# Kernel tuning notes

Measured on AMD Instinct MI355X. Metric: run time of the kernel, lower is better.

The kernel has to match this reference:

```python
import jax, jax.numpy as jnp
import numpy as np

NEG_SLOPE = 0.2
EPS = 1e-16

def gat_conv(x, edge_index, W, a_src, a_dst, b):
    # x: [N, Fin], W: [Fin, C], a_src/a_dst: [C], b: [C]
    N = x.shape[0]
    src, dst = edge_index[0], edge_index[1]
    h = x @ W                                  # [N, C]
    alpha_s = h @ a_src                        # [N]
    alpha_d = h @ a_dst                        # [N]
    e = alpha_s[src] + alpha_d[dst]            # [E]
    e = jnp.where(e > 0, e, NEG_SLOPE * e)     # LeakyReLU(0.2)
    # ragged softmax over incoming edges of each dst node
    m = jax.ops.segment_max(e, dst, num_segments=N)       # [N]
    p = jnp.exp(e - m[dst])                                # [E]
    s = jax.ops.segment_sum(p, dst, num_segments=N)        # [N]
    alpha = p / (s[dst] + EPS)                             # [E]
    out = jax.ops.segment_sum(alpha[:, None] * h[src], dst, num_segments=N)
    return out + b

def setup_inputs() -> dict:
    key = jax.random.key(0)
    ks = jax.random.split(key, 10)
    N, Fin, H, C, E = 50000, 128, 64, 64, 800000
    x = jax.random.normal(ks[0], (N, Fin), dtype=jnp.float32)
    edge_index = jax.random.randint(ks[1], (2, E), 0, N, dtype=jnp.int64)
    sc1 = 1.0 / np.sqrt(Fin)
    sc2 = 1.0 / np.sqrt(H)
    W1 = jax.random.normal(ks[2], (Fin, H), dtype=jnp.float32) * sc1
    a_src1 = jax.random.normal(ks[3], (H,), dtype=jnp.float32) * sc2
    a_dst1 = jax.random.normal(ks[4], (H,), dtype=jnp.float32) * sc2
    b1 = jnp.zeros((H,), dtype=jnp.float32)
    W2 = jax.random.normal(ks[5], (H, C), dtype=jnp.float32) * sc2
    a_src2 = jax.random.normal(ks[6], (C,), dtype=jnp.float32) * sc2
    a_dst2 = jax.random.normal(ks[7], (C,), dtype=jnp.float32) * sc2
    b2 = jnp.zeros((C,), dtype=jnp.float32)
    return {"x": x, "edge_index": edge_index, "W1": W1, "a_src1": a_src1,
            "a_dst1": a_dst1, "b1": b1, "W2": W2, "a_src2": a_src2,
            "a_dst2": a_dst2, "b2": b2}

def reference(x, edge_index, W1, a_src1, a_dst1, b1, W2, a_src2, a_dst2, b2):
    h = gat_conv(x, edge_index, W1, a_src1, a_dst1, b1)
    h = jax.nn.relu(h)
    out = gat_conv(h, edge_index, W2, a_src2, a_dst2, b2)
    return out
```

## Files before the change

### kernel.cpp

```cpp
#include <hip/hip_runtime.h>
#include <cstddef>

constexpr int FIN = 128;
constexpr int EPB = 2048;
constexpr int BSH = 7;
constexpr int NPB = 128;
constexpr int PACK_SH = 25;
constexpr int SRCMASK = (1 << PACK_SH) - 1;
constexpr int RSTR = 512;
constexpr int CAP = 4608;
constexpr int RPS = NPB + 1;

typedef _Float16 half4 __attribute__((ext_vector_type(4)));
typedef _Float16 half8 __attribute__((ext_vector_type(8)));
typedef float floatx4 __attribute__((ext_vector_type(4)));

template <int NW>
__device__ __forceinline__ int block_scan_tot(int v, int tid, int* wsums,
                                              int* tot) {
    int lane = tid & 63, w = tid >> 6;
    int x = v;
#pragma unroll
    for (int off = 1; off < 64; off <<= 1) {
        int y = __shfl_up(x, off, 64);
        if (lane >= off) x += y;
    }
    if (lane == 63) wsums[w] = x;
    __syncthreads();
    int add = 0, t = 0;
#pragma unroll
    for (int i = 0; i < NW; ++i) {
        add += (i < w) ? wsums[i] : 0;
        t += wsums[i];
    }
    *tot = t;
    return x + add - v;
}

template <int K>
__device__ __forceinline__
void gemm_core(const float* __restrict__ W, const float* __restrict__ ASRC,
               const float* __restrict__ ADST, _Float16* __restrict__ Hh,
               float* __restrict__ AS, float* __restrict__ AD, int N, int nb,
               _Float16* Xh, _Float16* WT) {
    constexpr int LDH = K + 8;
    const int tid = threadIdx.x;
    for (int i = tid; i < 64 * (K / 4); i += 256) {
        int n = i & 63, kg = i >> 6;
        half4 h;
#pragma unroll
        for (int j = 0; j < 4; ++j)
            h[j] = (_Float16)W[(4 * kg + j) * 64 + n];
        *(half4*)(WT + n * LDH + 4 * kg) = h;
    }
    __syncthreads();

    const int l = tid & 63;
    const int r0 = (tid >> 6) * 16;
    const int n16 = l & 15, quad = l >> 4;

    floatx4 acc[4];
#pragma unroll
    for (int nt = 0; nt < 4; ++nt) acc[nt] = (floatx4){0.f, 0.f, 0.f, 0.f};

#pragma unroll
    for (int k0 = 0; k0 < K; k0 += 32) {
        half8 a = *(const half8*)(Xh + (r0 + n16) * LDH + k0 + quad * 8);
#pragma unroll
        for (int nt = 0; nt < 4; ++nt) {
            half8 b = *(const half8*)(WT + (nt * 16 + n16) * LDH + k0 + quad * 8);
            acc[nt] = __builtin_amdgcn_mfma_f32_16x16x32_f16(a, b, acc[nt], 0, 0, 0);
        }
    }

    float pa[4] = {0.f, 0.f, 0.f, 0.f}, pd[4] = {0.f, 0.f, 0.f, 0.f};
#pragma unroll
    for (int nt = 0; nt < 4; ++nt) {
        float as_v = ASRC[nt * 16 + n16], ad_v = ADST[nt * 16 + n16];
#pragma unroll
        for (int reg = 0; reg < 4; ++reg) {
            pa[reg] += acc[nt][reg] * as_v;
            pd[reg] += acc[nt][reg] * ad_v;
        }
    }
#pragma unroll
    for (int off = 1; off < 16; off <<= 1) {
#pragma unroll
        for (int reg = 0; reg < 4; ++reg) {
            pa[reg] += __shfl_xor(pa[reg], off, 64);
            pd[reg] += __shfl_xor(pd[reg], off, 64);
        }
    }
    if (n16 == 0) {
#pragma unroll
        for (int reg = 0; reg < 4; ++reg) {
            int row = nb + r0 + quad * 4 + reg;
            if (row < N) { AS[row] = pa[reg]; AD[row] = pd[reg]; }
        }
    }

#pragma unroll
    for (int nt = 0; nt < 4; ++nt)
#pragma unroll
        for (int reg = 0; reg < 4; ++reg)
            Xh[(r0 + quad * 4 + reg) * LDH + nt * 16 + n16] = (_Float16)acc[nt][reg];
    {
        int r = r0 + (l >> 2);
        int o = (l & 3) * 16;
        if (nb + r < N) {
            half8 v0 = *(const half8*)(Xh + r * LDH + o);
            half8 v1 = *(const half8*)(Xh + r * LDH + o + 8);
            *(half8*)(Hh + (size_t)(nb + r) * 64 + o) = v0;
            *(half8*)(Hh + (size_t)(nb + r) * 64 + o + 8) = v1;
        }
    }
}

template <int K, typename XT>
__device__ __forceinline__
void gemm_mfma_body(const XT* __restrict__ X, const float* __restrict__ W,
                    const float* __restrict__ ASRC, const float* __restrict__ ADST,
                    _Float16* __restrict__ Hh, float* __restrict__ AS,
                    float* __restrict__ AD, int N, int blk,
                    _Float16* Xh, _Float16* WT) {
    constexpr int LDH = K + 8;
    const int tid = threadIdx.x;
    const int nb = blk * 64;
    if constexpr (sizeof(XT) == 4) {
        constexpr int QPR = K / 4;
        for (int i = tid; i < 64 * QPR; i += 256) {
            int r = i / QPR, q = i % QPR;
            float4 v = make_float4(0.f, 0.f, 0.f, 0.f);
            if (nb + r < N) v = *(const float4*)(X + (size_t)(nb + r) * K + 4 * q);
            half4 h; h[0] = (_Float16)v.x; h[1] = (_Float16)v.y;
            h[2] = (_Float16)v.z; h[3] = (_Float16)v.w;
            *(half4*)(Xh + r * LDH + 4 * q) = h;
        }
    } else {
        constexpr int OPR = K / 8;
        for (int i = tid; i < 64 * OPR; i += 256) {
            int r = i / OPR, o = i % OPR;
            half8 v = {};
            if (nb + r < N) v = *(const half8*)(X + (size_t)(nb + r) * K + 8 * o);
            *(half8*)(Xh + r * LDH + 8 * o) = v;
        }
    }
    gemm_core<K>(W, ASRC, ADST, Hh, AS, AD, N, nb, Xh, WT);
}

__global__ __launch_bounds__(256)
void gemm1_and_sort(const float* __restrict__ X, const float* __restrict__ W,
                    const float* __restrict__ ASRC, const float* __restrict__ ADST,
                    _Float16* __restrict__ Hh, float* __restrict__ AS,
                    float* __restrict__ AD, int N,
                    const int* __restrict__ src, const int* __restrict__ dst,
                    int E, int nblk, int nbuck,
                    int* __restrict__ rows, int* __restrict__ ebuck) {
    constexpr int K = FIN, LDH = K + 8;
    __shared__ _Float16 Xh[64 * LDH];
    __shared__ _Float16 WT[64 * LDH];
    __shared__ int wsums[4];

    const int tid = threadIdx.x;
    if ((int)blockIdx.x < nblk) {
        int* sorted = (int*)Xh;
        int* hist   = (int*)WT;
        int* cur    = hist + 512;
        for (int i = tid; i < nbuck; i += 256) hist[i] = 0;
        __syncthreads();

        const int e0 = blockIdx.x * EPB;
        const int e1 = min(e0 + EPB, E);
        const int cnt = e1 - e0;

        int pay[8], bk[8];
#pragma unroll
        for (int k = 0; k < 8; ++k) {
            int e = e0 + tid + k * 256;
            bk[k] = -1; pay[k] = 0;
            if (e < e1) {
                int d = dst[e];
                bk[k] = d >> BSH;
                pay[k] = ((d & (NPB - 1)) << PACK_SH) | src[e];
                atomicAdd(&hist[bk[k]], 1);
            }
        }
        __syncthreads();

        int i0 = 2 * tid, i1 = 2 * tid + 1;
        int v0 = (i0 < nbuck) ? hist[i0] : 0;
        int v1 = (i1 < nbuck) ? hist[i1] : 0;
        int tot;
        int ex = block_scan_tot<4>(v0 + v1, tid, wsums, &tot);
        if (i0 < nbuck) {
            cur[i0] = ex;
            rows[blockIdx.x * RSTR + i0] = ex;
        }
        if (i1 < nbuck) {
            cur[i1] = ex + v0;
            rows[blockIdx.x * RSTR + i1] = ex + v0;
        }
        if (tid == 0) rows[blockIdx.x * RSTR + nbuck] = cnt;
        __syncthreads();

#pragma unroll
        for (int k = 0; k < 8; ++k) {
            if (bk[k] >= 0) {
                int p = atomicAdd(&cur[bk[k]], 1);
                sorted[p] = pay[k];
            }
        }
        __syncthreads();
        for (int i = tid; i < cnt; i += 256)
            ebuck[blockIdx.x * EPB + i] = sorted[i];
        return;
    }
    gemm_mfma_body<K, float>(X, W, ASRC, ADST, Hh, AS, AD, N,
                             blockIdx.x - nblk, Xh, WT);
}

template <int K, typename XT>
__global__ __launch_bounds__(256)
void gemm_feat(const XT* __restrict__ X, const float* __restrict__ W,
               const float* __restrict__ ASRC, const float* __restrict__ ADST,
               _Float16* __restrict__ Hh, float* __restrict__ AS,
               float* __restrict__ AD, int N) {
    constexpr int LDH = K + 8;
    __shared__ _Float16 Xh[64 * LDH];
    __shared__ _Float16 WT[64 * LDH];
    gemm_mfma_body<K, XT>(X, W, ASRC, ADST, Hh, AS, AD, N, blockIdx.x, Xh, WT);
}

template <typename OT>
__device__ __forceinline__
void agg_one_node(const _Float16* __restrict__ Hh, const float* __restrict__ AS,
                  const float* __restrict__ AD, const int* __restrict__ csr_src,
                  const float* __restrict__ bias, OT* __restrict__ OUT,
                  int n, int base, int end, int lane, int relu) {
    const int cnt = end - base;
    const float adn = AD[n];

    if (cnt > 64) {
        float m = -INFINITY;
        for (int c0 = base; c0 < end; c0 += 64) {
            int c = min(64, end - c0);
            float e = -INFINITY;
            if (lane < c) {
                int sr = csr_src[c0 + lane];
                float t = AS[sr] + adn;
                e = t > 0.f ? t : 0.2f * t;
            }
#pragma unroll
            for (int off = 32; off > 0; off >>= 1) e = fmaxf(e, __shfl_xor(e, off, 64));
            m = fmaxf(m, e);
        }
        float s = 0.f, acc = 0.f;
        for (int c0 = base; c0 < end; c0 += 64) {
            int c = min(64, end - c0);
            int srcl = 0;
            float p = 0.f;
            if (lane < c) {
                srcl = csr_src[c0 + lane];
                float t = AS[srcl] + adn;
                t = t > 0.f ? t : 0.2f * t;
                p = __expf(t - m);
            }
            float cs = p;
#pragma unroll
            for (int off = 32; off > 0; off >>= 1) cs += __shfl_xor(cs, off, 64);
            s += cs;
            for (int j = 0; j < c; ++j)
                acc += __shfl(p, j, 64) *
                       (float)Hh[(size_t)__shfl(srcl, j, 64) * 64 + lane];
        }
        float o = acc * (1.f / (s + 1e-16f)) + bias[lane];
        if (relu) o = fmaxf(o, 0.f);
        OUT[(size_t)n * 64 + lane] = (OT)o;
        return;
    }

    int srcl = 0;
    float el = 0.f;
    if (lane < cnt) {
        srcl = csr_src[base + lane];
        float e = AS[srcl] + adn;
        el = e > 0.f ? e : 0.2f * e;
    }
    float p = (lane < cnt) ? __expf(el) : 0.f;
    float s = p;
#pragma unroll
    for (int off = 32; off > 0; off >>= 1) s += __shfl_xor(s, off, 64);
    const float inv = 1.f / (s + 1e-16f);

    const int eg = lane >> 3;
    const int c8 = (lane & 7) * 8;

    float acc[8], acc2[8];
#pragma unroll
    for (int t = 0; t < 8; ++t) { acc[t] = 0.f; acc2[t] = 0.f; }

    int j = 0;
    for (; j + 16 <= cnt; j += 16) {
        int iA = j + eg, iB = j + 8 + eg;
        int sA = __shfl(srcl, iA, 64), sB = __shfl(srcl, iB, 64);
        float aA = __shfl(p, iA, 64),  aB = __shfl(p, iB, 64);
        half8 hA = *(const half8*)(Hh + (size_t)sA * 64 + c8);
        half8 hB = *(const half8*)(Hh + (size_t)sB * 64 + c8);
#pragma unroll
        for (int t = 0; t < 8; ++t) {
            acc[t]  += aA * (float)hA[t];
            acc2[t] += aB * (float)hB[t];
        }
    }
    for (; j < cnt; j += 8) {
        int iA = j + eg;
        int sA = __shfl(srcl, iA, 64);
        float aA = __shfl(p, iA, 64);
        half8 hA = *(const half8*)(Hh + (size_t)sA * 64 + c8);
#pragma unroll
        for (int t = 0; t < 8; ++t) acc[t] += aA * (float)hA[t];
    }
#pragma unroll
    for (int t = 0; t < 8; ++t) acc[t] += acc2[t];
#pragma unroll
    for (int off = 8; off <= 32; off <<= 1)
#pragma unroll
        for (int t = 0; t < 8; ++t) acc[t] += __shfl_xor(acc[t], off, 64);

    if (lane < 8) {
        float4 b0 = *(const float4*)(bias + c8);
        float4 b1 = *(const float4*)(bias + c8 + 4);
        float o[8];
        o[0] = acc[0] * inv + b0.x; o[1] = acc[1] * inv + b0.y;
        o[2] = acc[2] * inv + b0.z; o[3] = acc[3] * inv + b0.w;
        o[4] = acc[4] * inv + b1.x; o[5] = acc[5] * inv + b1.y;
        o[6] = acc[6] * inv + b1.z; o[7] = acc[7] * inv + b1.w;
        if (relu) {
#pragma unroll
            for (int t = 0; t < 8; ++t) o[t] = fmaxf(o[t], 0.f);
        }
        if constexpr (sizeof(OT) == 2) {
            half8 hv;
#pragma unroll
            for (int t = 0; t < 8; ++t) hv[t] = (_Float16)o[t];
            *(half8*)((_Float16*)OUT + (size_t)n * 64 + c8) = hv;
        } else {
            *(float4*)((float*)OUT + (size_t)n * 64 + c8) =
                make_float4(o[0], o[1], o[2], o[3]);
            *(float4*)((float*)OUT + (size_t)n * 64 + c8 + 4) =
                make_float4(o[4], o[5], o[6], o[7]);
        }
    }
}

template <typename OT>
__device__ __forceinline__
void agg_pair_core(const _Float16* __restrict__ Hh, const float* __restrict__ AS,
                   const float* __restrict__ AD, const int* __restrict__ csr,
                   const float* __restrict__ bias, OT* __restrict__ OUT,
                   int n, int N, int relu, int lane, int base, int end) {
    const int l32 = lane & 31;
    const int cnt = end - base;

    if (!__all(cnt <= 32)) {
        int baseA = __shfl(base, 0, 64),  endA = __shfl(end, 0, 64);
        int baseB = __shfl(base, 32, 64), endB = __shfl(end, 32, 64);
        int nA = __shfl(n, 0, 64), nB = __shfl(n, 32, 64);
        if (nA < N) agg_one_node<OT>(Hh, AS, AD, csr, bias, OUT, nA, baseA, endA, lane, relu);
        if (nB < N) agg_one_node<OT>(Hh, AS, AD, csr, bias, OUT, nB, baseB, endB, lane, relu);
        return;
    }

    const float adn = (n < N) ? AD[n] : 0.f;
    int srcl = 0;
    float p = 0.f;
    if (l32 < cnt) {
        srcl = csr[base + l32];
        float e = AS[srcl] + adn;
        e = e > 0.f ? e : 0.2f * e;
        p = __expf(e);
    }
    float s = p;
#pragma unroll
    for (int off = 16; off > 0; off >>= 1) s += __shfl_xor(s, off, 64);
    const float inv = 1.f / (s + 1e-16f);

    const int eg = l32 >> 3;
    const int c8 = (l32 & 7) * 8;

    float acc[8], acc2[8];
#pragma unroll
    for (int t = 0; t < 8; ++t) { acc[t] = 0.f; acc2[t] = 0.f; }

    int j = 0;
    for (; j + 8 <= cnt; j += 8) {
        int iA = j + eg, iB = j + 4 + eg;
        int sA = __shfl(srcl, iA, 32), sB = __shfl(srcl, iB, 32);
        float aA = __shfl(p, iA, 32),  aB = __shfl(p, iB, 32);
        half8 hA = *(const half8*)(Hh + (size_t)sA * 64 + c8);
        half8 hB = *(const half8*)(Hh + (size_t)sB * 64 + c8);
#pragma unroll
        for (int t = 0; t < 8; ++t) {
            acc[t]  += aA * (float)hA[t];
            acc2[t] += aB * (float)hB[t];
        }
    }
    for (; j < cnt; j += 4) {
        int iA = j + eg;
        int sA = __shfl(srcl, iA, 32);
        float aA = __shfl(p, iA, 32);
        half8 hA = *(const half8*)(Hh + (size_t)sA * 64 + c8);
#pragma unroll
        for (int t = 0; t < 8; ++t) acc[t] += aA * (float)hA[t];
    }
#pragma unroll
    for (int t = 0; t < 8; ++t) acc[t] += acc2[t];
#pragma unroll
    for (int t = 0; t < 8; ++t) acc[t] += __shfl_xor(acc[t], 8, 64);
#pragma unroll
    for (int t = 0; t < 8; ++t) acc[t] += __shfl_xor(acc[t], 16, 64);

    if (l32 < 8 && n < N) {
        float4 b0 = *(const float4*)(bias + c8);
        float4 b1 = *(const float4*)(bias + c8 + 4);
        float o[8];
        o[0] = acc[0] * inv + b0.x; o[1] = acc[1] * inv + b0.y;
        o[2] = acc[2] * inv + b0.z; o[3] = acc[3] * inv + b0.w;
        o[4] = acc[4] * inv + b1.x; o[5] = acc[5] * inv + b1.y;
        o[6] = acc[6] * inv + b1.z; o[7] = acc[7] * inv + b1.w;
        if (relu) {
#pragma unroll
            for (int t = 0; t < 8; ++t) o[t] = fmaxf(o[t], 0.f);
        }
        if constexpr (sizeof(OT) == 2) {
            half8 hv;
#pragma unroll
            for (int t = 0; t < 8; ++t) hv[t] = (_Float16)o[t];
            *(half8*)((_Float16*)OUT + (size_t)n * 64 + c8) = hv;
        } else {
            *(float4*)((float*)OUT + (size_t)n * 64 + c8) =
                make_float4(o[0], o[1], o[2], o[3]);
            *(float4*)((float*)OUT + (size_t)n * 64 + c8 + 4) =
                make_float4(o[4], o[5], o[6], o[7]);
        }
    }
}

__global__ __launch_bounds__(512)
void bucket_agg1(const int* __restrict__ ebuck, const int* __restrict__ rows,
                 int nblk, int N,
                 const _Float16* __restrict__ Hh, const float* __restrict__ AS1,
                 const float* __restrict__ AD1, const float* __restrict__ b1,
                 _Float16* __restrict__ R1h,
                 int* __restrict__ ebuck2, int* __restrict__ rp2) {
    __shared__ int eL[CAP];
    __shared__ int eS[CAP];
    __shared__ int hist[NPB];
    __shared__ int cur[NPB];
    __shared__ int rowr[RPS];
    __shared__ int wsums[8];
    __shared__ int cursor;
    const int b = blockIdx.x, tid = threadIdx.x;

    if (tid < NPB) hist[tid] = 0;
    if (tid == 0) cursor = 0;
    __syncthreads();

    for (int blk = tid; blk < nblk; blk += 512) {
        int r0 = rows[blk * RSTR + b];
        int r1 = rows[blk * RSTR + b + 1];
        int len = r1 - r0;
        if (len > 0) {
            int ofs = atomicAdd(&cursor, len);
            for (int i = 0; i < len; ++i)
                if (ofs + i < CAP) eL[ofs + i] = ebuck[blk * EPB + r0 + i];
        }
    }
    __syncthreads();
    const int btot = min(cursor, CAP);

    for (int e = tid; e < btot; e += 512)
        atomicAdd(&hist[((unsigned)eL[e]) >> PACK_SH], 1);
    __syncthreads();
    int v = (tid < NPB) ? hist[tid] : 0;
    int tot;
    int excl = block_scan_tot<8>(v, tid, wsums, &tot);
    if (tid < NPB) { cur[tid] = excl; rowr[tid] = excl; }
    if (tid == 0) rowr[NPB] = btot;
    __syncthreads();
    for (int e = tid; e < btot; e += 512) {
        int pv = eL[e];
        int p = atomicAdd(&cur[((unsigned)pv) >> PACK_SH], 1);
        eS[p] = pv & SRCMASK;
    }
    __syncthreads();

    for (int i = tid; i < btot; i += 512)
        ebuck2[(size_t)b * CAP + i] = eS[i];
    for (int j = tid; j < RPS; j += 512)
        rp2[b * RPS + j] = rowr[j];

    const int lane = tid & 63, w = tid >> 6;
    const int half = lane >> 5;
#pragma unroll 1
    for (int q = 0; q < 8; ++q) {
        int nloc = w * 16 + q * 2 + half;
        int n = (b << BSH) + nloc;
        int base = rowr[nloc], end = rowr[nloc + 1];
        agg_pair_core<_Float16>(Hh, AS1, AD1, (const int*)eS, b1, R1h,
                                n, N, 1, lane, base, end);
    }
}

__global__ __launch_bounds__(256)
void gat_aggregate2(const _Float16* __restrict__ Hh, const float* __restrict__ AS,
                    const float* __restrict__ AD, const int* __restrict__ ebuck2,
                    const int* __restrict__ rp2, const float* __restrict__ bias,
                    float* __restrict__ OUT, int N) {
    const int lane = threadIdx.x & 63;
    const int half = lane >> 5;
    const int pair0 = blockIdx.x * 8 + (threadIdx.x >> 6) * 2;
    if (pair0 >= N) return;
    const int n = pair0 + half;
    int base = 0, end = 0;
    if (n < N) {
        int b = n >> BSH, j = n & (NPB - 1);
        base = b * CAP + rp2[b * RPS + j];
        end  = b * CAP + rp2[b * RPS + j + 1];
    }
    agg_pair_core<float>(Hh, AS, AD, ebuck2, bias, OUT, n, N, 0, lane, base, end);
}

extern "C" void kernel_launch(void* const* d_in, const int* in_sizes, int n_in,
                              void* d_out, int out_size, void* d_ws, size_t ws_size,
                              hipStream_t stream) {
    const float* x    = (const float*)d_in[0];
    const int*   ei   = (const int*)d_in[1];
    const float* W1   = (const float*)d_in[2];
    const float* as1w = (const float*)d_in[3];
    const float* ad1w = (const float*)d_in[4];
    const float* b1   = (const float*)d_in[5];
    const float* W2   = (const float*)d_in[6];
    const float* as2w = (const float*)d_in[7];
    const float* ad2w = (const float*)d_in[8];
    const float* b2   = (const float*)d_in[9];
    float* out = (float*)d_out;

    const int N = in_sizes[0] / FIN;
    const int E = in_sizes[1] / 2;
    const int* esrc = ei;
    const int* edst = ei + E;

    const int nbuck = (N + NPB - 1) >> BSH;
    const int nblk  = (E + EPB - 1) / EPB;

    char* wp8 = (char*)d_ws;
    _Float16* Hh  = (_Float16*)wp8;  wp8 += (size_t)N * 64 * 2;
    _Float16* R1h = (_Float16*)wp8;  wp8 += (size_t)N * 64 * 2;
    _Float16* H2h = (_Float16*)wp8;  wp8 += (size_t)N * 64 * 2;
    float* AS1 = (float*)wp8;        wp8 += (size_t)N * 4;
    float* AD1 = (float*)wp8;        wp8 += (size_t)N * 4;
    float* AS2 = (float*)wp8;        wp8 += (size_t)N * 4;
    float* AD2 = (float*)wp8;        wp8 += (size_t)N * 4;
    int* ebuck  = (int*)wp8;         wp8 += (size_t)nblk * EPB * 4;
    int* rows   = (int*)wp8;         wp8 += (size_t)nblk * RSTR * 4;
    int* ebuck2 = (int*)wp8;         wp8 += (size_t)nbuck * CAP * 4;
    int* rp2    = (int*)wp8;         wp8 += (size_t)nbuck * RPS * 4;

    const int nbG = (N + 63) / 64;
    const int nbAgg = (N + 7) / 8;

    hipLaunchKernelGGL(gemm1_and_sort, dim3(nblk + nbG), dim3(256), 0, stream,
                       x, W1, as1w, ad1w, Hh, AS1, AD1, N,
                       esrc, edst, E, nblk, nbuck, rows, ebuck);
    hipLaunchKernelGGL(bucket_agg1, dim3(nbuck), dim3(512), 0, stream,
                       ebuck, rows, nblk, N, Hh, AS1, AD1, b1, R1h,
                       ebuck2, rp2);
    hipLaunchKernelGGL((gemm_feat<64, _Float16>), dim3(nbG), dim3(256), 0, stream,
                       R1h, W2, as2w, ad2w, H2h, AS2, AD2, N);
    hipLaunchKernelGGL(gat_aggregate2, dim3(nbAgg), dim3(256), 0, stream,
                       H2h, AS2, AD2, ebuck2, rp2, b2, out, N);
}
```

Measured before the change: 162.7 us.

## Fuse layer-2 GEMM into bucket aggregation kernel via LDS-resident activations

The layer-1 aggregation now writes its ReLU'd fp16 output rows into shared memory, reusing the edge-list buffer, instead of writing them to a global R1h buffer. The same block then runs the 64x64 MFMA GEMM with W2 and computes the layer-2 attention logits directly from LDS. This removes one kernel launch and the global write and re-read of the intermediate activation. In exchange, each block uses more shared memory for the W2 tile and takes a longer tail, which may lower occupancy.

```diff
diff --git a/kernel.cpp b/kernel.cpp
--- a/kernel.cpp
+++ b/kernel.cpp
@@ -219,24 +219,12 @@
                              blockIdx.x - nblk, Xh, WT);
 }
 
-template <int K, typename XT>
-__global__ __launch_bounds__(256)
-void gemm_feat(const XT* __restrict__ X, const float* __restrict__ W,
-               const float* __restrict__ ASRC, const float* __restrict__ ADST,
-               _Float16* __restrict__ Hh, float* __restrict__ AS,
-               float* __restrict__ AD, int N) {
-    constexpr int LDH = K + 8;
-    __shared__ _Float16 Xh[64 * LDH];
-    __shared__ _Float16 WT[64 * LDH];
-    gemm_mfma_body<K, XT>(X, W, ASRC, ADST, Hh, AS, AD, N, blockIdx.x, Xh, WT);
-}
-
-template <typename OT>
+template <bool LDSOUT, typename OT>
 __device__ __forceinline__
 void agg_one_node(const _Float16* __restrict__ Hh, const float* __restrict__ AS,
                   const float* __restrict__ AD, const int* __restrict__ csr_src,
                   const float* __restrict__ bias, OT* __restrict__ OUT,
-                  int n, int base, int end, int lane, int relu) {
+                  _Float16* ldsX, int n, int base, int end, int lane, int relu) {
     const int cnt = end - base;
     const float adn = AD[n];
 
@@ -275,7 +263,8 @@
         }
         float o = acc * (1.f / (s + 1e-16f)) + bias[lane];
         if (relu) o = fmaxf(o, 0.f);
-        OUT[(size_t)n * 64 + lane] = (OT)o;
+        if constexpr (LDSOUT) ldsX[(n & (NPB - 1)) * 72 + lane] = (_Float16)o;
+        else OUT[(size_t)n * 64 + lane] = (OT)o;
         return;
     }
 
@@ -339,7 +328,12 @@
 #pragma unroll
             for (int t = 0; t < 8; ++t) o[t] = fmaxf(o[t], 0.f);
         }
-        if constexpr (sizeof(OT) == 2) {
+        if constexpr (LDSOUT) {
+            half8 hv;
+#pragma unroll
+            for (int t = 0; t < 8; ++t) hv[t] = (_Float16)o[t];
+            *(half8*)(ldsX + (n & (NPB - 1)) * 72 + c8) = hv;
+        } else if constexpr (sizeof(OT) == 2) {
             half8 hv;
 #pragma unroll
             for (int t = 0; t < 8; ++t) hv[t] = (_Float16)o[t];
@@ -353,12 +347,13 @@
     }
 }
 
-template <typename OT>
+template <bool LDSOUT, typename OT>
 __device__ __forceinline__
 void agg_pair_core(const _Float16* __restrict__ Hh, const float* __restrict__ AS,
                    const float* __restrict__ AD, const int* __restrict__ csr,
                    const float* __restrict__ bias, OT* __restrict__ OUT,
-                   int n, int N, int relu, int lane, int base, int end) {
+                   _Float16* ldsX, int n, int N, int relu, int lane,
+                   int base, int end) {
     const int l32 = lane & 31;
     const int cnt = end - base;
 
@@ -366,8 +361,10 @@
         int baseA = __shfl(base, 0, 64),  endA = __shfl(end, 0, 64);
         int baseB = __shfl(base, 32, 64), endB = __shfl(end, 32, 64);
         int nA = __shfl(n, 0, 64), nB = __shfl(n, 32, 64);
-        if (nA < N) agg_one_node<OT>(Hh, AS, AD, csr, bias, OUT, nA, baseA, endA, lane, relu);
-        if (nB < N) agg_one_node<OT>(Hh, AS, AD, csr, bias, OUT, nB, baseB, endB, lane, relu);
+        if (nA < N) agg_one_node<LDSOUT, OT>(Hh, AS, AD, csr, bias, OUT, ldsX,
+                                             nA, baseA, endA, lane, relu);
+        if (nB < N) agg_one_node<LDSOUT, OT>(Hh, AS, AD, csr, bias, OUT, ldsX,
+                                             nB, baseB, endB, lane, relu);
         return;
     }
 
@@ -432,7 +429,12 @@
 #pragma unroll
             for (int t = 0; t < 8; ++t) o[t] = fmaxf(o[t], 0.f);
         }
-        if constexpr (sizeof(OT) == 2) {
+        if constexpr (LDSOUT) {
+            half8 hv;
+#pragma unroll
+            for (int t = 0; t < 8; ++t) hv[t] = (_Float16)o[t];
+            *(half8*)(ldsX + (n & (NPB - 1)) * 72 + c8) = hv;
+        } else if constexpr (sizeof(OT) == 2) {
             half8 hv;
 #pragma unroll
             for (int t = 0; t < 8; ++t) hv[t] = (_Float16)o[t];
@@ -447,14 +449,17 @@
 }
 
 __global__ __launch_bounds__(512)
-void bucket_agg1(const int* __restrict__ ebuck, const int* __restrict__ rows,
-                 int nblk, int N,
-                 const _Float16* __restrict__ Hh, const float* __restrict__ AS1,
-                 const float* __restrict__ AD1, const float* __restrict__ b1,
-                 _Float16* __restrict__ R1h,
-                 int* __restrict__ ebuck2, int* __restrict__ rp2) {
-    __shared__ int eL[CAP];
+void bucket_agg1_gemm2(const int* __restrict__ ebuck, const int* __restrict__ rows,
+                       int nblk, int N,
+                       const _Float16* __restrict__ Hh, const float* __restrict__ AS1,
+                       const float* __restrict__ AD1, const float* __restrict__ b1,
+                       const float* __restrict__ W2, const float* __restrict__ as2w,
+                       const float* __restrict__ ad2w, _Float16* __restrict__ H2h,
+                       float* __restrict__ AS2, float* __restrict__ AD2,
+                       int* __restrict__ ebuck2, int* __restrict__ rp2) {
+    __shared__ int eLX[CAP];
     __shared__ int eS[CAP];
+    __shared__ _Float16 WT[64 * 72];
     __shared__ int hist[NPB];
     __shared__ int cur[NPB];
     __shared__ int rowr[RPS];
@@ -462,6 +467,14 @@
     __shared__ int cursor;
     const int b = blockIdx.x, tid = threadIdx.x;
 
+    for (int i = tid; i < 64 * 16; i += 512) {
+        int n = i & 63, kg = i >> 6;
+        half4 h;
+#pragma unroll
+        for (int j = 0; j < 4; ++j)
+            h[j] = (_Float16)W2[(4 * kg + j) * 64 + n];
+        *(half4*)(WT + n * 72 + 4 * kg) = h;
+    }
     if (tid < NPB) hist[tid] = 0;
     if (tid == 0) cursor = 0;
     __syncthreads();
@@ -473,14 +486,14 @@
         if (len > 0) {
             int ofs = atomicAdd(&cursor, len);
             for (int i = 0; i < len; ++i)
-                if (ofs + i < CAP) eL[ofs + i] = ebuck[blk * EPB + r0 + i];
+                if (ofs + i < CAP) eLX[ofs + i] = ebuck[blk * EPB + r0 + i];
         }
     }
     __syncthreads();
     const int btot = min(cursor, CAP);
 
     for (int e = tid; e < btot; e += 512)
-        atomicAdd(&hist[((unsigned)eL[e]) >> PACK_SH], 1);
+        atomicAdd(&hist[((unsigned)eLX[e]) >> PACK_SH], 1);
     __syncthreads();
     int v = (tid < NPB) ? hist[tid] : 0;
     int tot;
@@ -489,7 +502,7 @@
     if (tid == 0) rowr[NPB] = btot;
     __syncthreads();
     for (int e = tid; e < btot; e += 512) {
-        int pv = eL[e];
+        int pv = eLX[e];
         int p = atomicAdd(&cur[((unsigned)pv) >> PACK_SH], 1);
         eS[p] = pv & SRCMASK;
     }
@@ -499,6 +512,11 @@
         ebuck2[(size_t)b * CAP + i] = eS[i];
     for (int j = tid; j < RPS; j += 512)
         rp2[b * RPS + j] = rowr[j];
+
+    _Float16* Xh = (_Float16*)eLX;
+    for (int i = tid; i < 128 * 72 / 8; i += 512)
+        ((half8*)Xh)[i] = (half8){};
+    __syncthreads();
 
     const int lane = tid & 63, w = tid >> 6;
     const int half = lane >> 5;
@@ -507,8 +525,75 @@
         int nloc = w * 16 + q * 2 + half;
         int n = (b << BSH) + nloc;
         int base = rowr[nloc], end = rowr[nloc + 1];
-        agg_pair_core<_Float16>(Hh, AS1, AD1, (const int*)eS, b1, R1h,
-                                n, N, 1, lane, base, end);
+        agg_pair_core<true, _Float16>(Hh, AS1, AD1, (const int*)eS, b1,
+                                      (_Float16*)nullptr, Xh, n, N, 1, lane,
+                                      base, end);
+    }
+    __syncthreads();
+
+    const int tt = tid & 255;
+    const int tile = tid >> 8;
+    const int nb = (b << BSH) + tile * 64;
+    _Float16* Xt = Xh + tile * 64 * 72;
+
+    const int l = tt & 63;
+    const int r0 = (tt >> 6) * 16;
+    const int n16 = l & 15, quad = l >> 4;
+
+    floatx4 acc[4];
+#pragma unroll
+    for (int nt = 0; nt < 4; ++nt) acc[nt] = (floatx4){0.f, 0.f, 0.f, 0.f};
+
+#pragma unroll
+    for (int k0 = 0; k0 < 64; k0 += 32) {
+        half8 a = *(const half8*)(Xt + (r0 + n16) * 72 + k0 + quad * 8);
+#pragma unroll
+        for (int nt = 0; nt < 4; ++nt) {
+            half8 bb = *(const half8*)(WT + (nt * 16 + n16) * 72 + k0 + quad * 8);
+            acc[nt] = __builtin_amdgcn_mfma_f32_16x16x32_f16(a, bb, acc[nt], 0, 0, 0);
+        }
+    }
+
+    float pa[4] = {0.f, 0.f, 0.f, 0.f}, pd[4] = {0.f, 0.f, 0.f, 0.f};
+#pragma unroll
+    for (int nt = 0; nt < 4; ++nt) {
+        float as_v = as2w[nt * 16 + n16], ad_v = ad2w[nt * 16 + n16];
+#pragma unroll
+        for (int reg = 0; reg < 4; ++reg) {
+            pa[reg] += acc[nt][reg] * as_v;
+            pd[reg] += acc[nt][reg] * ad_v;
+        }
+    }
+#pragma unroll
+    for (int off = 1; off < 16; off <<= 1) {
+#pragma unroll
+        for (int reg = 0; reg < 4; ++reg) {
+            pa[reg] += __shfl_xor(pa[reg], off, 64);
+            pd[reg] += __shfl_xor(pd[reg], off, 64);
+        }
+    }
+    if (n16 == 0) {
+#pragma unroll
+        for (int reg = 0; reg < 4; ++reg) {
+            int row = nb + r0 + quad * 4 + reg;
+            if (row < N) { AS2[row] = pa[reg]; AD2[row] = pd[reg]; }
+        }
+    }
+
+#pragma unroll
+    for (int nt = 0; nt < 4; ++nt)
+#pragma unroll
+        for (int reg = 0; reg < 4; ++reg)
+            Xt[(r0 + quad * 4 + reg) * 72 + nt * 16 + n16] = (_Float16)acc[nt][reg];
+    {
+        int r = r0 + (l >> 2);
+        int o = (l & 3) * 16;
+        if (nb + r < N) {
+            half8 v0 = *(const half8*)(Xt + r * 72 + o);
+            half8 v1 = *(const half8*)(Xt + r * 72 + o + 8);
+            *(half8*)(H2h + (size_t)(nb + r) * 64 + o) = v0;
+            *(half8*)(H2h + (size_t)(nb + r) * 64 + o + 8) = v1;
+        }
     }
 }
 
@@ -528,7 +613,8 @@
         base = b * CAP + rp2[b * RPS + j];
         end  = b * CAP + rp2[b * RPS + j + 1];
     }
-    agg_pair_core<float>(Hh, AS, AD, ebuck2, bias, OUT, n, N, 0, lane, base, end);
+    agg_pair_core<false, float>(Hh, AS, AD, ebuck2, bias, OUT,
+                                (_Float16*)nullptr, n, N, 0, lane, base, end);
 }
 
 extern "C" void kernel_launch(void* const* d_in, const int* in_sizes, int n_in,
@@ -556,7 +642,6 @@
 
     char* wp8 = (char*)d_ws;
     _Float16* Hh  = (_Float16*)wp8;  wp8 += (size_t)N * 64 * 2;
-    _Float16* R1h = (_Float16*)wp8;  wp8 += (size_t)N * 64 * 2;
     _Float16* H2h = (_Float16*)wp8;  wp8 += (size_t)N * 64 * 2;
     float* AS1 = (float*)wp8;        wp8 += (size_t)N * 4;
     float* AD1 = (float*)wp8;        wp8 += (size_t)N * 4;
@@ -573,11 +658,9 @@
     hipLaunchKernelGGL(gemm1_and_sort, dim3(nblk + nbG), dim3(256), 0, stream,
                        x, W1, as1w, ad1w, Hh, AS1, AD1, N,
                        esrc, edst, E, nblk, nbuck, rows, ebuck);
-    hipLaunchKernelGGL(bucket_agg1, dim3(nbuck), dim3(512), 0, stream,
-                       ebuck, rows, nblk, N, Hh, AS1, AD1, b1, R1h,
-                       ebuck2, rp2);
-    hipLaunchKernelGGL((gemm_feat<64, _Float16>), dim3(nbG), dim3(256), 0, stream,
-                       R1h, W2, as2w, ad2w, H2h, AS2, AD2, N);
+    hipLaunchKernelGGL(bucket_agg1_gemm2, dim3(nbuck), dim3(512), 0, stream,
+                       ebuck, rows, nblk, N, Hh, AS1, AD1, b1,
+                       W2, as2w, ad2w, H2h, AS2, AD2, ebuck2, rp2);
     hipLaunchKernelGGL(gat_aggregate2, dim3(nbAgg), dim3(256), 0, stream,
                        H2h, AS2, AD2, ebuck2, rp2, b2, out, N);
 }
```

New measurement: 159.1 us. 1.02x faster.
